# Kernel optimization log

Measured on AMD Instinct MI355X. Metric: run time of the kernel, lower is better.

## Reference

```python
import jax, jax.numpy as jnp
import numpy as np

B, S, D, H = 2, 2048, 1024, 16
DK = D // H  # 64


def setup_inputs() -> dict:
    key = jax.random.key(0)
    ks = jax.random.split(key, 11)
    std = 1.0 / np.sqrt(D)
    inp = {
        "q": jax.random.normal(ks[0], (B, S, D), jnp.float32),
        "k": jax.random.normal(ks[1], (B, S, D), jnp.float32),
        "v": jax.random.normal(ks[2], (B, S, D), jnp.float32),
        # causal mask: True means masked (matches masked_fill(mask == True, -1e9))
        "mask": jnp.triu(jnp.ones((1, 1, S, S), dtype=bool), k=1),
        "Wq": jax.random.normal(ks[3], (D, D), jnp.float32) * std,
        "bq": jnp.zeros((D,), jnp.float32),
        "Wk": jax.random.normal(ks[4], (D, D), jnp.float32) * std,
        "bk": jnp.zeros((D,), jnp.float32),
        "Wv": jax.random.normal(ks[5], (D, D), jnp.float32) * std,
        "bv": jnp.zeros((D,), jnp.float32),
        "Wo": jax.random.normal(ks[6], (D, D), jnp.float32) * std,
        "bo": jnp.zeros((D,), jnp.float32),
    }
    return inp


def _split_heads(x):
    b, s, _ = x.shape
    return x.reshape(b, s, H, DK).transpose(0, 2, 1, 3)  # [B,H,S,DK]


def reference(q, k, v, mask, Wq, bq, Wk, bk, Wv, bv, Wo, bo):
    # QKV projections (nn.Linear: x @ W.T + b)
    qh = _split_heads(q @ Wq.T + bq)
    kh = _split_heads(k @ Wk.T + bk)
    vh = _split_heads(v @ Wv.T + bv)
    # scaled dot-product attention (dropout is identity in eval)
    scores = jnp.einsum("bhqd,bhkd->bhqk", qh, kh) / jnp.sqrt(
        jnp.asarray(DK, jnp.float32))
    scores = jnp.where(mask, jnp.float32(-1e9), scores)
    attn = jax.nn.softmax(scores, axis=-1)
    out = jnp.einsum("bhqk,bhkd->bhqd", attn, vh)
    # combine heads [B,H,S,DK] -> [B,S,D], then output projection
    out = out.transpose(0, 2, 1, 3).reshape(q.shape[0], -1, D)
    return out @ Wo.T + bo
```

## Files before the change

### kernel.cpp

```cpp
#include <hip/hip_runtime.h>
#include <stdint.h>

#define S_LEN 2048
#define DMODEL 1024
#define NHEAD 16
#define DKH 64

typedef __attribute__((ext_vector_type(8))) short short8;
typedef __attribute__((ext_vector_type(4))) short sv4;
typedef __attribute__((ext_vector_type(4))) float fv4;
typedef __attribute__((ext_vector_type(8))) __bf16 bf16x8;
typedef __attribute__((ext_vector_type(4))) float f32x4;

#define QSCALE 0.18033688011112042f

static __device__ __forceinline__ short f2bf(float f) {
  unsigned u = __builtin_bit_cast(unsigned, f);
  u = u + 0x7fffu + ((u >> 16) & 1u);
  return (short)(u >> 16);
}

static __device__ __forceinline__ bf16x8 ldfrag(const void* p) {
  return __builtin_bit_cast(bf16x8, *(const short8*)p);
}

#define GLL16(gp, lp) __builtin_amdgcn_global_load_lds( \
    (const __attribute__((address_space(1))) unsigned int*)(const void*)(gp), \
    (__attribute__((address_space(3))) unsigned int*)(void*)(lp), 16, 0, 0)

#define WAIT_VMCNT0() asm volatile("s_waitcnt vmcnt(0)" ::: "memory")
#define WAIT_LGKM0()  asm volatile("s_waitcnt lgkmcnt(0)" ::: "memory")

__global__ __launch_bounds__(256) void convert_all(
    const float* __restrict__ q, const float* __restrict__ k, const float* __restrict__ v,
    const float* __restrict__ wq, const float* __restrict__ wk, const float* __restrict__ wv,
    const float* __restrict__ wo,
    short* __restrict__ xb, short* __restrict__ wb, short* __restrict__ wob)
{
  const int total = 4194304;
  for (int gid = blockIdx.x * blockDim.x + threadIdx.x; gid < total;
       gid += gridDim.x * blockDim.x) {
    const float* src; short* dst; int off; float scl = 1.0f;
    if (gid < 3145728) {
      int z = gid >> 20;
      off = (gid & 1048575) << 2;
      src = (z == 0) ? q : (z == 1) ? k : v;
      dst = xb + (size_t)z * 4194304;
    } else {
      int g = gid - 3145728;
      int z = g >> 18;
      off = (g & 262143) << 2;
      src = (z == 0) ? wq : (z == 1) ? wk : (z == 2) ? wv : wo;
      dst = (z < 3) ? (wb + (size_t)z * 1048576) : wob;
      if (z == 0) scl = QSCALE;
    }
    fv4 f = *(const fv4*)(src + off);
    sv4 o;
    o.x = f2bf(f.x * scl); o.y = f2bf(f.y * scl);
    o.z = f2bf(f.z * scl); o.w = f2bf(f.w * scl);
    *(sv4*)(dst + off) = o;
  }
}

__global__ __launch_bounds__(256) void gemm_bt(
    const short* __restrict__ Abase, const short* __restrict__ Wbase,
    const float* __restrict__ bias0, const float* __restrict__ bias1,
    const float* __restrict__ bias2, float bscl0,
    short* __restrict__ Cbf, float* __restrict__ Cf)
{
  const int Kd = 1024, Nd = 1024, Md = 4096;
  const int z = blockIdx.z;
  const short* A = Abase + (size_t)z * Md * Kd;
  const short* W = Wbase + (size_t)z * Nd * Kd;
  const float* bias = (z == 0) ? bias0 : (z == 1) ? bias1 : bias2;
  const float bscl = (z == 0) ? bscl0 : 1.0f;

  __shared__ short8 AB[2048];
  short8* As = AB;
  short8* Bs = AB + 1024;

  const int tid = threadIdx.x;
  const int w = tid >> 6, lane = tid & 63;
  const int wr = w >> 1, wc = w & 1;
  const int lhi = lane >> 4, llo = lane & 15;
  const int m0 = blockIdx.y * 128, n0 = blockIdx.x * 128;

  const f32x4 zero = {0.f, 0.f, 0.f, 0.f};
  f32x4 acc[4][4];
#pragma unroll
  for (int i = 0; i < 4; ++i)
#pragma unroll
    for (int j = 0; j < 4; ++j) acc[i][j] = zero;

  for (int kt = 0; kt < Kd / 64; ++kt) {
    const int k0 = kt * 64;
    __syncthreads();
#pragma unroll
    for (int inst = 0; inst < 4; ++inst) {
      int ib = w * 4096 + inst * 1024 + lane * 16;
      int row = ib >> 7;
      int colb = (ib & 127) ^ ((row & 7) << 4);
      int col = colb >> 1;
      GLL16(A + (size_t)(m0 + row) * Kd + k0 + col,
            (char*)As + (w * 4096 + inst * 1024));
      GLL16(W + (size_t)(n0 + row) * Kd + k0 + col,
            (char*)Bs + (w * 4096 + inst * 1024));
    }
    __syncthreads();
#pragma unroll
    for (int kk = 0; kk < 2; ++kk) {
      bf16x8 af[4], bfm[4];
#pragma unroll
      for (int t = 0; t < 4; ++t) {
        int arow = wr * 64 + t * 16 + llo;
        int abyte = ((arow << 7) + ((kk * 32 + lhi * 8) << 1)) ^ ((arow & 7) << 4);
        af[t] = ldfrag((const char*)As + abyte);
        int brow = wc * 64 + t * 16 + llo;
        int bbyte = ((brow << 7) + ((kk * 32 + lhi * 8) << 1)) ^ ((brow & 7) << 4);
        bfm[t] = ldfrag((const char*)Bs + bbyte);
      }
#pragma unroll
      for (int i = 0; i < 4; ++i)
#pragma unroll
        for (int j = 0; j < 4; ++j)
          acc[i][j] = __builtin_amdgcn_mfma_f32_16x16x32_bf16(af[i], bfm[j], acc[i][j], 0, 0, 0);
    }
  }

  if (Cbf) {
    short* Co = Cbf + (size_t)z * Md * Nd;
    __syncthreads();
    short* Cs = (short*)AB;
#pragma unroll
    for (int i = 0; i < 4; ++i) {
#pragma unroll
      for (int j = 0; j < 4; ++j) {
        int col = wc * 64 + j * 16 + llo;
        float bv_ = bias[n0 + col] * bscl;
#pragma unroll
        for (int r = 0; r < 4; ++r) {
          int row = wr * 64 + i * 16 + lhi * 4 + r;
          Cs[row * 128 + col] = f2bf(acc[i][j][r] + bv_);
        }
      }
    }
    __syncthreads();
#pragma unroll
    for (int s = 0; s < 8; ++s) {
      int lb = s * 4096 + tid * 16;
      short8 vL = *(const short8*)((const char*)Cs + lb);
      int row = lb >> 8;
      int colb = lb & 255;
      *(short8*)&Co[(size_t)(m0 + row) * Nd + n0 + (colb >> 1)] = vL;
    }
  } else {
#pragma unroll
    for (int i = 0; i < 4; ++i) {
#pragma unroll
      for (int j = 0; j < 4; ++j) {
#pragma unroll
        for (int r = 0; r < 4; ++r) {
          int row = m0 + wr * 64 + i * 16 + lhi * 4 + r;
          int col = n0 + wc * 64 + j * 16 + llo;
          Cf[(size_t)row * Nd + col] = acc[i][j][r] + bias[col] * bscl;
        }
      }
    }
  }
}

__global__ __launch_bounds__(256) void attn_fwd(
    const short* __restrict__ Qp, const short* __restrict__ Kp,
    const short* __restrict__ Vp, short* __restrict__ Out)
{
  __shared__ short8 Ks[2][512];
  __shared__ short  Vt[64 * 72];
  __shared__ short  PsA[4][16 * 72];

  const int tid = threadIdx.x;
  const int w = tid >> 6, lane = tid & 63;
  const int lhi = lane >> 4, llo = lane & 15;

  const int id = blockIdx.x;
  const int g  = id & 255;
  const int kq = id >> 8;
  const int wv = g & 7;
  const int bh = g >> 3;
  const int qt = (kq == 0) ? 2 * wv : (kq == 1) ? 31 - 2 * wv
               : (kq == 2) ? 2 * wv + 1 : 30 - 2 * wv;
  const int nt = qt + 1;
  const int qbase = qt * 64;
  const int b = bh >> 4, h = bh & 15;
  const size_t rowbase = (size_t)b * S_LEN;
  const short* Kbase = Kp + rowbase * DMODEL + h * DKH;
  const short* Vbase = Vp + rowbase * DMODEL + h * DKH;

  short* Ps = PsA[w];
  const f32x4 zero = {0.f, 0.f, 0.f, 0.f};

  bf16x8 qf[2];
  {
    const short* qrow = Qp + (rowbase + qbase + w * 16 + llo) * DMODEL + h * DKH;
    qf[0] = ldfrag(qrow + lhi * 8);
    qf[1] = ldfrag(qrow + 32 + lhi * 8);
  }

  float mr[4], lr[4];
  f32x4 oacc[4];
#pragma unroll
  for (int r = 0; r < 4; ++r) { mr[r] = -3.0e38f; lr[r] = 0.f; }
#pragma unroll
  for (int dt = 0; dt < 4; ++dt) oacc[dt] = zero;

  const int kvs = lane, dgrp = w;

#pragma unroll
  for (int inst = 0; inst < 2; ++inst) {
    int ib = w * 2048 + inst * 1024 + lane * 16;
    int row = ib >> 7;
    int colb = (ib & 127) ^ ((row & 7) << 4);
    GLL16(Kbase + (size_t)row * DMODEL + (colb >> 1),
          (char*)&Ks[0][0] + (w * 2048 + inst * 1024));
  }
  short8 va, vb;
  va = *(const short8*)(Vbase + (size_t)kvs * DMODEL + dgrp * 16);
  vb = *(const short8*)(Vbase + (size_t)kvs * DMODEL + dgrp * 16 + 8);

  for (int t = 0; t < nt; ++t) {
    const int cur = t & 1, nxt = cur ^ 1;
    const int kvbase = t * 64;

    WAIT_VMCNT0();
#pragma unroll
    for (int j = 0; j < 8; ++j) Vt[(dgrp * 16 + j) * 72 + kvs] = va[j];
#pragma unroll
    for (int j = 0; j < 8; ++j) Vt[(dgrp * 16 + 8 + j) * 72 + kvs] = vb[j];
    if (t + 1 < nt) {
      const int nb = kvbase + 64;
#pragma unroll
      for (int inst = 0; inst < 2; ++inst) {
        int ib = w * 2048 + inst * 1024 + lane * 16;
        int row = ib >> 7;
        int colb = (ib & 127) ^ ((row & 7) << 4);
        GLL16(Kbase + (size_t)(nb + row) * DMODEL + (colb >> 1),
              (char*)&Ks[nxt][0] + (w * 2048 + inst * 1024));
      }
      va = *(const short8*)(Vbase + (size_t)(nb + kvs) * DMODEL + dgrp * 16);
      vb = *(const short8*)(Vbase + (size_t)(nb + kvs) * DMODEL + dgrp * 16 + 8);
    }
    WAIT_LGKM0();
    __builtin_amdgcn_s_barrier();

    f32x4 sc[4];
#pragma unroll
    for (int tt = 0; tt < 4; ++tt) sc[tt] = zero;
    __builtin_amdgcn_s_setprio(1);
#pragma unroll
    for (int kk = 0; kk < 2; ++kk) {
#pragma unroll
      for (int tt = 0; tt < 4; ++tt) {
        int krow = tt * 16 + llo;
        int kbyte = ((krow << 7) + ((kk * 32 + lhi * 8) << 1)) ^ ((krow & 7) << 4);
        bf16x8 kf = ldfrag((const char*)&Ks[cur][0] + kbyte);
        sc[tt] = __builtin_amdgcn_mfma_f32_16x16x32_bf16(qf[kk], kf, sc[tt], 0, 0, 0);
      }
    }
    __builtin_amdgcn_s_setprio(0);

    const bool diag = (t == qt);
    float sv[4][4], tmx[4];
#pragma unroll
    for (int r = 0; r < 4; ++r) {
#pragma unroll
      for (int tt = 0; tt < 4; ++tt) {
        float s = sc[tt][r];
        if (diag) {
          int kg = kvbase + tt * 16 + llo;
          int qg = qbase + w * 16 + lhi * 4 + r;
          if (kg > qg) s = -3.0e38f;
        }
        sv[tt][r] = s;
      }
      float trm = fmaxf(fmaxf(sv[0][r], sv[1][r]), fmaxf(sv[2][r], sv[3][r]));
      trm = fmaxf(trm, __shfl_xor(trm, 1));
      trm = fmaxf(trm, __shfl_xor(trm, 2));
      trm = fmaxf(trm, __shfl_xor(trm, 4));
      trm = fmaxf(trm, __shfl_xor(trm, 8));
      tmx[r] = trm;
    }
    bool grow = (tmx[0] > mr[0] + 8.f) || (tmx[1] > mr[1] + 8.f) ||
                (tmx[2] > mr[2] + 8.f) || (tmx[3] > mr[3] + 8.f);
    if (__ballot(grow)) {
#pragma unroll
      for (int r = 0; r < 4; ++r) {
        float mnew = fmaxf(mr[r], tmx[r]);
        float alpha = __builtin_amdgcn_exp2f(mr[r] - mnew);
        mr[r] = mnew;
        lr[r] *= alpha;
#pragma unroll
        for (int dt = 0; dt < 4; ++dt) oacc[dt][r] = oacc[dt][r] * alpha;
      }
    }
#pragma unroll
    for (int r = 0; r < 4; ++r) {
      float rs = 0.f;
#pragma unroll
      for (int tt = 0; tt < 4; ++tt) {
        float pv = __builtin_amdgcn_exp2f(sv[tt][r] - mr[r]);
        rs += pv;
        Ps[(lhi * 4 + r) * 72 + tt * 16 + llo] = f2bf(pv);
      }
      rs += __shfl_xor(rs, 1);
      rs += __shfl_xor(rs, 2);
      rs += __shfl_xor(rs, 4);
      rs += __shfl_xor(rs, 8);
      lr[r] += rs;
    }

    __builtin_amdgcn_s_setprio(1);
#pragma unroll
    for (int kk = 0; kk < 2; ++kk) {
      bf16x8 pa = ldfrag(Ps + llo * 72 + kk * 32 + lhi * 8);
#pragma unroll
      for (int dt = 0; dt < 4; ++dt) {
        bf16x8 vf = ldfrag(&Vt[(dt * 16 + llo) * 72 + kk * 32 + lhi * 8]);
        oacc[dt] = __builtin_amdgcn_mfma_f32_16x16x32_bf16(pa, vf, oacc[dt], 0, 0, 0);
      }
    }
    __builtin_amdgcn_s_setprio(0);
    __builtin_amdgcn_s_barrier();
  }

#pragma unroll
  for (int dt = 0; dt < 4; ++dt)
#pragma unroll
    for (int r = 0; r < 4; ++r)
      Ps[(lhi * 4 + r) * 64 + dt * 16 + llo] = f2bf(oacc[dt][r] / lr[r]);
  WAIT_LGKM0();
#pragma unroll
  for (int s = 0; s < 2; ++s) {
    int lb = lane * 32 + s * 16;
    short8 vL = *(const short8*)((const char*)Ps + lb);
    int row = lb >> 7;
    int colb = lb & 127;
    *(short8*)&Out[(rowbase + qbase + w * 16 + row) * DMODEL + h * DKH + (colb >> 1)] = vL;
  }
}

extern "C" void kernel_launch(void* const* d_in, const int* in_sizes, int n_in,
                              void* d_out, int out_size, void* d_ws, size_t ws_size,
                              hipStream_t stream) {
  (void)in_sizes; (void)n_in; (void)out_size; (void)ws_size;
  const float* q  = (const float*)d_in[0];
  const float* k  = (const float*)d_in[1];
  const float* v  = (const float*)d_in[2];
  const float* Wq = (const float*)d_in[4];
  const float* bq = (const float*)d_in[5];
  const float* Wk = (const float*)d_in[6];
  const float* bk = (const float*)d_in[7];
  const float* Wv = (const float*)d_in[8];
  const float* bv = (const float*)d_in[9];
  const float* Wo = (const float*)d_in[10];
  const float* bo = (const float*)d_in[11];
  float* out = (float*)d_out;

  short* xb   = (short*)d_ws;
  short* wb   = xb + 3ull * 4194304;
  short* wob  = wb + 3ull * 1048576;
  short* proj = wob + 1048576;
  short* attno = xb;

  convert_all<<<dim3(2048), dim3(256), 0, stream>>>(q, k, v, Wq, Wk, Wv, Wo, xb, wb, wob);
  gemm_bt<<<dim3(8, 32, 3), dim3(256), 0, stream>>>(xb, wb, bq, bk, bv, QSCALE, proj, nullptr);
  attn_fwd<<<dim3(1024), dim3(256), 0, stream>>>(proj, proj + 4194304ull,
                                                 proj + 2ull * 4194304, attno);
  gemm_bt<<<dim3(8, 32, 1), dim3(256), 0, stream>>>(attno, wob, bo, bo, bo, 1.0f, nullptr, out);
}
```

Baseline: 282.2 us.

## Split projection GEMMs, retile output GEMM, swizzle block order, defer row-sum reduction

Splits the shared GEMM into a bf16-output projection kernel and a dedicated fp32 output-projection kernel. The output GEMM uses 128x64 tiles, giving 512 blocks instead of 256 so more compute units stay busy. Both GEMMs remap block indices with a grouped swizzle meant to improve L2 reuse of A and W tiles. In attention, the per-iteration cross-lane row-sum shuffles move to a single reduction at the end. The output is now written straight from registers rather than staged through LDS, which gives narrower, less coalesced stores.

```diff
diff --git a/kernel.cpp b/kernel.cpp
--- a/kernel.cpp
+++ b/kernel.cpp
@@ -62,11 +62,11 @@
   }
 }
 
-__global__ __launch_bounds__(256) void gemm_bt(
+__global__ __launch_bounds__(256) void gemm_proj(
     const short* __restrict__ Abase, const short* __restrict__ Wbase,
     const float* __restrict__ bias0, const float* __restrict__ bias1,
     const float* __restrict__ bias2, float bscl0,
-    short* __restrict__ Cbf, float* __restrict__ Cf)
+    short* __restrict__ Cbf)
 {
   const int Kd = 1024, Nd = 1024, Md = 4096;
   const int z = blockIdx.z;
@@ -83,7 +83,9 @@
   const int w = tid >> 6, lane = tid & 63;
   const int wr = w >> 1, wc = w & 1;
   const int lhi = lane >> 4, llo = lane & 15;
-  const int m0 = blockIdx.y * 128, n0 = blockIdx.x * 128;
+  const int id = blockIdx.x + 8 * blockIdx.y;
+  const int sw = (id & 7) * 32 + (id >> 3);
+  const int n0 = (sw & 7) * 128, m0 = (sw >> 3) * 128;
 
   const f32x4 zero = {0.f, 0.f, 0.f, 0.f};
   f32x4 acc[4][4];
@@ -127,43 +129,110 @@
     }
   }
 
-  if (Cbf) {
-    short* Co = Cbf + (size_t)z * Md * Nd;
+  short* Co = Cbf + (size_t)z * Md * Nd;
+  __syncthreads();
+  short* Cs = (short*)AB;
+#pragma unroll
+  for (int i = 0; i < 4; ++i) {
+#pragma unroll
+    for (int j = 0; j < 4; ++j) {
+      int col = wc * 64 + j * 16 + llo;
+      float bv_ = bias[n0 + col] * bscl;
+#pragma unroll
+      for (int r = 0; r < 4; ++r) {
+        int row = wr * 64 + i * 16 + lhi * 4 + r;
+        Cs[row * 128 + col] = f2bf(acc[i][j][r] + bv_);
+      }
+    }
+  }
+  __syncthreads();
+#pragma unroll
+  for (int s = 0; s < 8; ++s) {
+    int lb = s * 4096 + tid * 16;
+    short8 vL = *(const short8*)((const char*)Cs + lb);
+    int row = lb >> 8;
+    int colb = lb & 255;
+    *(short8*)&Co[(size_t)(m0 + row) * Nd + n0 + (colb >> 1)] = vL;
+  }
+}
+
+__global__ __launch_bounds__(256) void gemm_out(
+    const short* __restrict__ A, const short* __restrict__ W,
+    const float* __restrict__ bias, float* __restrict__ Cf)
+{
+  const int Kd = 1024, Nd = 1024;
+
+  __shared__ short8 As[1024];
+  __shared__ short8 Bs[512];
+
+  const int tid = threadIdx.x;
+  const int w = tid >> 6, lane = tid & 63;
+  const int wr = w >> 1, wc = w & 1;
+  const int lhi = lane >> 4, llo = lane & 15;
+  const int id = blockIdx.x + 16 * blockIdx.y;
+  const int sw = (id & 7) * 64 + (id >> 3);
+  const int n0 = (sw & 15) * 64, m0 = (sw >> 4) * 128;
+
+  const f32x4 zero = {0.f, 0.f, 0.f, 0.f};
+  f32x4 acc[4][2];
+#pragma unroll
+  for (int i = 0; i < 4; ++i)
+#pragma unroll
+    for (int j = 0; j < 2; ++j) acc[i][j] = zero;
+
+  for (int kt = 0; kt < Kd / 64; ++kt) {
+    const int k0 = kt * 64;
     __syncthreads();
-    short* Cs = (short*)AB;
-#pragma unroll
-    for (int i = 0; i < 4; ++i) {
-#pragma unroll
-      for (int j = 0; j < 4; ++j) {
-        int col = wc * 64 + j * 16 + llo;
-        float bv_ = bias[n0 + col] * bscl;
-#pragma unroll
-        for (int r = 0; r < 4; ++r) {
-          int row = wr * 64 + i * 16 + lhi * 4 + r;
-          Cs[row * 128 + col] = f2bf(acc[i][j][r] + bv_);
-        }
-      }
+#pragma unroll
+    for (int inst = 0; inst < 4; ++inst) {
+      int ib = w * 4096 + inst * 1024 + lane * 16;
+      int row = ib >> 7;
+      int colb = (ib & 127) ^ ((row & 7) << 4);
+      GLL16(A + (size_t)(m0 + row) * Kd + k0 + (colb >> 1),
+            (char*)As + (w * 4096 + inst * 1024));
+    }
+#pragma unroll
+    for (int inst = 0; inst < 2; ++inst) {
+      int ib = w * 2048 + inst * 1024 + lane * 16;
+      int row = ib >> 7;
+      int colb = (ib & 127) ^ ((row & 7) << 4);
+      GLL16(W + (size_t)(n0 + row) * Kd + k0 + (colb >> 1),
+            (char*)Bs + (w * 2048 + inst * 1024));
     }
     __syncthreads();
 #pragma unroll
-    for (int s = 0; s < 8; ++s) {
-      int lb = s * 4096 + tid * 16;
-      short8 vL = *(const short8*)((const char*)Cs + lb);
-      int row = lb >> 8;
-      int colb = lb & 255;
-      *(short8*)&Co[(size_t)(m0 + row) * Nd + n0 + (colb >> 1)] = vL;
-    }
-  } else {
-#pragma unroll
-    for (int i = 0; i < 4; ++i) {
-#pragma unroll
-      for (int j = 0; j < 4; ++j) {
-#pragma unroll
-        for (int r = 0; r < 4; ++r) {
-          int row = m0 + wr * 64 + i * 16 + lhi * 4 + r;
-          int col = n0 + wc * 64 + j * 16 + llo;
-          Cf[(size_t)row * Nd + col] = acc[i][j][r] + bias[col] * bscl;
-        }
+    for (int kk = 0; kk < 2; ++kk) {
+      bf16x8 af[4], bfm[2];
+#pragma unroll
+      for (int t = 0; t < 4; ++t) {
+        int arow = wr * 64 + t * 16 + llo;
+        int abyte = ((arow << 7) + ((kk * 32 + lhi * 8) << 1)) ^ ((arow & 7) << 4);
+        af[t] = ldfrag((const char*)As + abyte);
+      }
+#pragma unroll
+      for (int j = 0; j < 2; ++j) {
+        int brow = wc * 32 + j * 16 + llo;
+        int bbyte = ((brow << 7) + ((kk * 32 + lhi * 8) << 1)) ^ ((brow & 7) << 4);
+        bfm[j] = ldfrag((const char*)Bs + bbyte);
+      }
+#pragma unroll
+      for (int i = 0; i < 4; ++i)
+#pragma unroll
+        for (int j = 0; j < 2; ++j)
+          acc[i][j] = __builtin_amdgcn_mfma_f32_16x16x32_bf16(af[i], bfm[j], acc[i][j], 0, 0, 0);
+    }
+  }
+
+#pragma unroll
+  for (int i = 0; i < 4; ++i) {
+#pragma unroll
+    for (int j = 0; j < 2; ++j) {
+      int col = n0 + wc * 32 + j * 16 + llo;
+      float bv_ = bias[col];
+#pragma unroll
+      for (int r = 0; r < 4; ++r) {
+        int row = m0 + wr * 64 + i * 16 + lhi * 4 + r;
+        Cf[(size_t)row * Nd + col] = acc[i][j][r] + bv_;
       }
     }
   }
@@ -310,10 +379,6 @@
         rs += pv;
         Ps[(lhi * 4 + r) * 72 + tt * 16 + llo] = f2bf(pv);
       }
-      rs += __shfl_xor(rs, 1);
-      rs += __shfl_xor(rs, 2);
-      rs += __shfl_xor(rs, 4);
-      rs += __shfl_xor(rs, 8);
       lr[r] += rs;
     }
 
@@ -332,18 +397,23 @@
   }
 
 #pragma unroll
-  for (int dt = 0; dt < 4; ++dt)
-#pragma unroll
-    for (int r = 0; r < 4; ++r)
-      Ps[(lhi * 4 + r) * 64 + dt * 16 + llo] = f2bf(oacc[dt][r] / lr[r]);
-  WAIT_LGKM0();
-#pragma unroll
-  for (int s = 0; s < 2; ++s) {
-    int lb = lane * 32 + s * 16;
-    short8 vL = *(const short8*)((const char*)Ps + lb);
-    int row = lb >> 7;
-    int colb = lb & 127;
-    *(short8*)&Out[(rowbase + qbase + w * 16 + row) * DMODEL + h * DKH + (colb >> 1)] = vL;
+  for (int r = 0; r < 4; ++r) {
+    float rs = lr[r];
+    rs += __shfl_xor(rs, 1);
+    rs += __shfl_xor(rs, 2);
+    rs += __shfl_xor(rs, 4);
+    rs += __shfl_xor(rs, 8);
+    lr[r] = rs;
+  }
+#pragma unroll
+  for (int dt = 0; dt < 4; ++dt) {
+#pragma unroll
+    for (int r = 0; r < 4; ++r) {
+      float vv = oacc[dt][r] / lr[r];
+      int row = qbase + w * 16 + lhi * 4 + r;
+      int col = h * DKH + dt * 16 + llo;
+      Out[(rowbase + row) * DMODEL + col] = f2bf(vv);
+    }
   }
 }
 
@@ -371,8 +441,8 @@
   short* attno = xb;
 
   convert_all<<<dim3(2048), dim3(256), 0, stream>>>(q, k, v, Wq, Wk, Wv, Wo, xb, wb, wob);
-  gemm_bt<<<dim3(8, 32, 3), dim3(256), 0, stream>>>(xb, wb, bq, bk, bv, QSCALE, proj, nullptr);
+  gemm_proj<<<dim3(8, 32, 3), dim3(256), 0, stream>>>(xb, wb, bq, bk, bv, QSCALE, proj);
   attn_fwd<<<dim3(1024), dim3(256), 0, stream>>>(proj, proj + 4194304ull,
                                                  proj + 2ull * 4194304, attno);
-  gemm_bt<<<dim3(8, 32, 1), dim3(256), 0, stream>>>(attno, wob, bo, bo, bo, 1.0f, nullptr, out);
-}
+  gemm_out<<<dim3(16, 32), dim3(256), 0, stream>>>(attno, wob, bo, out);
+}
```

New measurement: 256.4 us. 1.1x faster.
